# Kernel tuning notes

Measured on AMD Instinct MI355X. Metric: run time of the kernel, lower is better.

## Reference

```python
import jax, jax.numpy as jnp
import numpy as np

D_MODEL = 1024
NUM_HEADS = 16
D_HEAD = D_MODEL // NUM_HEADS
B, T = 2, 2048


def setup_inputs() -> dict:
    key = jax.random.key(0)
    kx, kq, kk, kv, ko = jax.random.split(key, 5)
    # xavier_uniform bound for square (D,D) linear weights
    bound = float(np.sqrt(6.0 / (D_MODEL + D_MODEL)))
    uni = lambda k: jax.random.uniform(k, (D_MODEL, D_MODEL), jnp.float32, -bound, bound)
    return {
        "x": jax.random.normal(kx, (B, T, D_MODEL), jnp.float32),
        "Wq": uni(kq),
        "Wk": uni(kk),
        "Wv": uni(kv),
        "Wo": uni(ko),
    }


def _split_heads(x):
    # (B, T, D) -> (B, H, T, d_head)
    b, t, _ = x.shape
    return x.reshape(b, t, NUM_HEADS, D_HEAD).transpose(0, 2, 1, 3)


def _exclusive_output_mod(Y, V):
    dt = V.dtype
    tiny = jnp.asarray(jnp.finfo(dt).tiny, dt)
    eps = jnp.asarray(jnp.finfo(dt).eps, dt)
    v_sq = jnp.sum(V * V, axis=-1, keepdims=True)
    y_dot_v = jnp.sum(Y * V, axis=-1, keepdims=True)
    scale = jnp.where(v_sq > 0, y_dot_v / jnp.maximum(v_sq, tiny), jnp.zeros_like(y_dot_v))
    Z = Y - scale * V
    residual_norm = jnp.linalg.norm(Z, axis=-1, keepdims=True)
    reference_norm = jnp.maximum(
        jnp.linalg.norm(Y, axis=-1, keepdims=True),
        jnp.linalg.norm(V, axis=-1, keepdims=True),
    )
    cleanup_tol = eps * Z.shape[-1] * reference_norm
    return jnp.where((v_sq > 0) & (residual_norm <= cleanup_tol), jnp.zeros_like(Z), Z)


def reference(x, Wq, Wk, Wv, Wo):
    Q = _split_heads(x @ Wq.T)  # (B,H,T,dh)
    K = _split_heads(x @ Wk.T)
    V = _split_heads(x @ Wv.T)
    sm_scale = 1.0 / np.sqrt(D_HEAD)
    scores = jnp.einsum("bhqd,bhkd->bhqk", Q, K) * sm_scale
    P = jax.nn.softmax(scores, axis=-1)
    Y = jnp.einsum("bhqk,bhkd->bhqd", P, V)
    Z = _exclusive_output_mod(Y, V)
    # merge heads: (B,H,T,dh) -> (B,T,D)
    Zm = Z.transpose(0, 2, 1, 3).reshape(x.shape[0], x.shape[1], D_MODEL)
    return Zm @ Wo.T
```

## Files before the change

### kernel.cpp

```cpp
#include <hip/hip_runtime.h>
#include <math.h>

#define DM   1024
#define TTOK 2048
#define NTOK 4096

typedef __bf16 bf16x8 __attribute__((ext_vector_type(8)));
typedef __bf16 bf16x4 __attribute__((ext_vector_type(4)));
typedef float  f32x4  __attribute__((ext_vector_type(4)));

#define QSCALE 0.18033688011112042f

#if defined(__has_builtin)
#if __has_builtin(__builtin_amdgcn_exp2f)
#define EXP2F(x) __builtin_amdgcn_exp2f(x)
#endif
#endif
#ifndef EXP2F
#define EXP2F(x) exp2f(x)
#endif

#define GLDS16(g, l) __builtin_amdgcn_global_load_lds( \
    (__attribute__((address_space(1))) void*)(g),      \
    (__attribute__((address_space(3))) void*)(l), 16, 0, 0)

__device__ __forceinline__ float qsum(float v) {
    v += __shfl_xor(v, 16, 64);
    v += __shfl_xor(v, 32, 64);
    return v;
}

__global__ __launch_bounds__(256)
void cvt_all(const float* __restrict__ x,  const float* __restrict__ Wq,
             const float* __restrict__ Wk, const float* __restrict__ Wv,
             const float* __restrict__ Wo, __bf16* __restrict__ dst) {
    size_t g = ((size_t)blockIdx.x * 256 + threadIdx.x) * 8;
    const float* s;
    size_t off;
    const size_t NX = (size_t)NTOK * DM;
    if (g < NX) { s = x; off = g; }
    else {
        size_t gg = g - NX;
        int w = (int)(gg >> 20);
        off = gg & ((1u << 20) - 1);
        s = (w == 0) ? Wq : (w == 1) ? Wk : (w == 2) ? Wv : Wo;
        off += 0;
    }
    float4 a = *(const float4*)(s + off);
    float4 b = *(const float4*)(s + off + 4);
    bf16x8 v;
    v[0] = (__bf16)a.x; v[1] = (__bf16)a.y; v[2] = (__bf16)a.z; v[3] = (__bf16)a.w;
    v[4] = (__bf16)b.x; v[5] = (__bf16)b.y; v[6] = (__bf16)b.z; v[7] = (__bf16)b.w;
    *(bf16x8*)(dst + g) = v;
}

template<int MODE>
__global__ __launch_bounds__(256)
void gemm_bf16(const __bf16* __restrict__ A,
               const __bf16* __restrict__ W0, const __bf16* __restrict__ W1,
               const __bf16* __restrict__ W2,
               __bf16* __restrict__ Oq, __bf16* __restrict__ Ok,
               __bf16* __restrict__ Ovt, float* __restrict__ Of)
{
    const int z = (MODE == 0) ? blockIdx.z : 0;
    const __bf16* W = (z == 0) ? W0 : (z == 1) ? W1 : W2;

    __shared__ __attribute__((aligned(16))) __bf16 As[128 * 32];
    __shared__ __attribute__((aligned(16))) __bf16 Bs[128 * 32];

    const int tid  = threadIdx.x;
    const int lane = tid & 63;
    const int wave = tid >> 6;
    const int wm = wave & 1, wn = wave >> 1;
    const int col = lane & 15, quad = lane >> 4;
    const int m0 = blockIdx.y * 128, n0 = blockIdx.x * 128;

    const __bf16* Ag = A + (size_t)(m0 + (tid >> 2)) * DM + (tid & 3) * 8;
    const __bf16* Wg = W + (size_t)(n0 + (tid >> 2)) * DM + (tid & 3) * 8;
    __bf16* lA = As + tid * 8;
    __bf16* lB = Bs + tid * 8;

    f32x4 acc[4][4];
#pragma unroll
    for (int i = 0; i < 4; ++i)
#pragma unroll
        for (int j = 0; j < 4; ++j)
#pragma unroll
            for (int r = 0; r < 4; ++r) acc[i][j][r] = 0.0f;

    for (int k0 = 0; k0 < DM; k0 += 32) {
        __syncthreads();
        GLDS16(Ag + k0,                   lA);
        GLDS16(Ag + (size_t)64 * DM + k0, lA + 2048);
        GLDS16(Wg + k0,                   lB);
        GLDS16(Wg + (size_t)64 * DM + k0, lB + 2048);
        __syncthreads();
        bf16x8 af[4], bfr[4];
#pragma unroll
        for (int i = 0; i < 4; ++i)
            af[i] = *(const bf16x8*)&As[(wm * 64 + i * 16 + col) * 32 + quad * 8];
#pragma unroll
        for (int j = 0; j < 4; ++j)
            bfr[j] = *(const bf16x8*)&Bs[(wn * 64 + j * 16 + col) * 32 + quad * 8];
#pragma unroll
        for (int i = 0; i < 4; ++i)
#pragma unroll
            for (int j = 0; j < 4; ++j)
                acc[i][j] = __builtin_amdgcn_mfma_f32_16x16x32_bf16(af[i], bfr[j], acc[i][j], 0, 0, 0);
    }

#pragma unroll
    for (int i = 0; i < 4; ++i) {
#pragma unroll
        for (int j = 0; j < 4; ++j) {
            const int mb = m0 + wm * 64 + i * 16 + quad * 4;
            const int n  = n0 + wn * 64 + j * 16 + col;
            if (MODE == 1) {
#pragma unroll
                for (int r = 0; r < 4; ++r)
                    Of[(size_t)(mb + r) * DM + n] = acc[i][j][r];
            } else {
                const int b = mb >> 11, t = mb & 2047;
                const int h = n >> 6,  d = n & 63;
                if (z == 2) {
                    bf16x4 pk;
#pragma unroll
                    for (int r = 0; r < 4; ++r) pk[r] = (__bf16)acc[i][j][r];
                    *(bf16x4*)&Ovt[(((size_t)(b * 16 + h)) * 64 + d) * TTOK + t] = pk;
                } else {
                    __bf16* dst = ((z == 0) ? Oq : Ok) +
                                  ((((size_t)(b * 16 + h)) * TTOK + t) * 64 + d);
                    const float sc = (z == 0) ? QSCALE : 1.0f;
#pragma unroll
                    for (int r = 0; r < 4; ++r) dst[(size_t)r * 64] = (__bf16)(acc[i][j][r] * sc);
                }
            }
        }
    }
}

__global__ __launch_bounds__(512)
void attn_mfma(const __bf16* __restrict__ Qg, const __bf16* __restrict__ Kg,
               const __bf16* __restrict__ Vtg, __bf16* __restrict__ Zm)
{
    const int bh = blockIdx.y;
    const int q0 = blockIdx.x * 128;
    const size_t base = (size_t)bh * TTOK * 64;

    __shared__ __attribute__((aligned(16))) __bf16 Ks[64 * 72];
    __shared__ __attribute__((aligned(16))) __bf16 Vs[64 * 72];
    __shared__ __attribute__((aligned(16))) __bf16 QPs[128 * 72];

    const int tid  = threadIdx.x;
    const int lane = tid & 63, wave = tid >> 6;
    const int col  = lane & 15, quad = lane >> 4;

#pragma unroll
    for (int it = 0; it < 2; ++it) {
        int c = tid + 512 * it;
        int r = c >> 3, off = (c & 7) * 8;
        *(bf16x8*)&QPs[r * 72 + off] =
            *(const bf16x8*)(Qg + base + (size_t)(q0 + r) * 64 + off);
    }
    __syncthreads();
    bf16x8 qf[2];
#pragma unroll
    for (int ks = 0; ks < 2; ++ks)
        qf[ks] = *(const bf16x8*)&QPs[(wave * 16 + col) * 72 + ks * 32 + quad * 8];

    bf16x8 ones;
#pragma unroll
    for (int i = 0; i < 8; ++i) ones[i] = (__bf16)1.0f;

    f32x4 O[4], lacc;
#pragma unroll
    for (int r = 0; r < 4; ++r) {
        lacc[r] = 0.0f;
#pragma unroll
        for (int nd = 0; nd < 4; ++nd) O[nd][r] = 0.0f;
    }

    const int rs = tid >> 3, offs = (tid & 7) * 8;

    for (int kb = 0; kb < TTOK / 64; ++kb) {
        bf16x8 kreg = *(const bf16x8*)(Kg + base + (size_t)(kb * 64 + rs) * 64 + offs);
        bf16x8 vreg = *(const bf16x8*)(Vtg + base + (size_t)rs * TTOK + kb * 64 + offs);
        __syncthreads();
        *(bf16x8*)&Ks[rs * 72 + offs] = kreg;
        *(bf16x8*)&Vs[rs * 72 + offs] = vreg;
        __syncthreads();

        f32x4 s[4];
#pragma unroll
        for (int nk = 0; nk < 4; ++nk)
#pragma unroll
            for (int r = 0; r < 4; ++r) s[nk][r] = 0.0f;
#pragma unroll
        for (int ks = 0; ks < 2; ++ks) {
            bf16x8 kf[4];
#pragma unroll
            for (int nk = 0; nk < 4; ++nk)
                kf[nk] = *(const bf16x8*)&Ks[(nk * 16 + col) * 72 + ks * 32 + quad * 8];
#pragma unroll
            for (int nk = 0; nk < 4; ++nk)
                s[nk] = __builtin_amdgcn_mfma_f32_16x16x32_bf16(kf[nk], qf[ks], s[nk], 0, 0, 0);
        }

#pragma unroll
        for (int nk = 0; nk < 4; ++nk) {
            float p0 = EXP2F(s[nk][0]);
            float p1 = EXP2F(s[nk][1]);
            float p2 = EXP2F(s[nk][2]);
            float p3 = EXP2F(s[nk][3]);
            bf16x4 pk;
            pk[0] = (__bf16)p0; pk[1] = (__bf16)p1;
            pk[2] = (__bf16)p2; pk[3] = (__bf16)p3;
            *(bf16x4*)&QPs[(wave * 16 + col) * 72 + nk * 16 + quad * 4] = pk;
        }

#pragma unroll
        for (int ks = 0; ks < 2; ++ks) {
            bf16x8 pf = *(const bf16x8*)&QPs[(wave * 16 + col) * 72 + ks * 32 + quad * 8];
            lacc = __builtin_amdgcn_mfma_f32_16x16x32_bf16(ones, pf, lacc, 0, 0, 0);
#pragma unroll
            for (int nd = 0; nd < 4; ++nd) {
                bf16x8 vf = *(const bf16x8*)&Vs[(nd * 16 + col) * 72 + ks * 32 + quad * 8];
                O[nd] = __builtin_amdgcn_mfma_f32_16x16x32_bf16(vf, pf, O[nd], 0, 0, 0);
            }
        }
    }

    const float inv = 1.0f / lacc[0];

    const int b = bh >> 4, h = bh & 15;
    const int q = q0 + wave * 16 + col;
    float y[4][4], vq[4][4];
    float yv = 0.f, v2 = 0.f, yy = 0.f;
#pragma unroll
    for (int nd = 0; nd < 4; ++nd)
#pragma unroll
        for (int r = 0; r < 4; ++r) {
            int d = nd * 16 + quad * 4 + r;
            float yval = O[nd][r] * inv;
            float vval = (float)Vtg[base + (size_t)d * TTOK + q];
            y[nd][r] = yval; vq[nd][r] = vval;
            yv += yval * vval; v2 += vval * vval; yy += yval * yval;
        }
    yv = qsum(yv); v2 = qsum(v2); yy = qsum(yy);
    float scl = (v2 > 0.0f) ? yv / fmaxf(v2, 1.1754943508222875e-38f) : 0.0f;
    float zz = 0.f;
    float zv[4][4];
#pragma unroll
    for (int nd = 0; nd < 4; ++nd)
#pragma unroll
        for (int r = 0; r < 4; ++r) {
            zv[nd][r] = y[nd][r] - scl * vq[nd][r];
            zz += zv[nd][r] * zv[nd][r];
        }
    zz = qsum(zz);
    float znorm = sqrtf(zz);
    float refn  = fmaxf(sqrtf(yy), sqrtf(v2));
    bool  wipe  = (v2 > 0.0f) && (znorm <= 1.1920928955078125e-07f * 64.0f * refn);
#pragma unroll
    for (int nd = 0; nd < 4; ++nd) {
        bf16x4 pk;
#pragma unroll
        for (int r = 0; r < 4; ++r) pk[r] = (__bf16)(wipe ? 0.0f : zv[nd][r]);
        *(bf16x4*)&Zm[((size_t)(b * TTOK + q)) * DM + h * 64 + nd * 16 + quad * 4] = pk;
    }
}

extern "C" void kernel_launch(void* const* d_in, const int* in_sizes, int n_in,
                              void* d_out, int out_size, void* d_ws, size_t ws_size,
                              hipStream_t stream) {
    const float* x  = (const float*)d_in[0];
    const float* Wq = (const float*)d_in[1];
    const float* Wk = (const float*)d_in[2];
    const float* Wv = (const float*)d_in[3];
    const float* Wo = (const float*)d_in[4];

    const size_t NX = (size_t)NTOK * DM;
    const size_t NW = (size_t)DM * DM;
    __bf16* xb  = (__bf16*)d_ws;
    __bf16* wqb = xb  + NX;
    __bf16* wkb = wqb + NW;
    __bf16* wvb = wkb + NW;
    __bf16* wob = wvb + NW;
    __bf16* Qb  = wob + NW;
    __bf16* Kb  = Qb  + NX;
    __bf16* Vtb = Kb  + NX;
    __bf16* Zmb = Vtb + NX;

    cvt_all<<<(NX + 4 * NW) / 2048, 256, 0, stream>>>(x, Wq, Wk, Wv, Wo, xb);

    gemm_bf16<0><<<dim3(DM / 128, NTOK / 128, 3), 256, 0, stream>>>(
        xb, wqb, wkb, wvb, Qb, Kb, Vtb, nullptr);

    attn_mfma<<<dim3(TTOK / 128, 32), 512, 0, stream>>>(Qb, Kb, Vtb, Zmb);

    gemm_bf16<1><<<dim3(DM / 128, NTOK / 128, 1), 256, 0, stream>>>(
        Zmb, wob, wob, wob, nullptr, nullptr, nullptr, (float*)d_out);
}
```

Before: 200.1 us.

## Switch attention to 32x32 MFMA with K/V prefetch and swap GEMM operands

The attention kernel moves from 16x16x32 to 32x32x16 bf16 MFMA, with 4 waves of 32 query rows each instead of 8 waves of 16. It register-prefetches the next K/V tile during compute, and it captures each query's own V row from shared memory when that tile passes, replacing a strided global gather in the epilogue. The Q/K projection and output GEMMs swap operands so the weight matrix is the M side, which gives contiguous vector stores (bf16x4 and float4) in place of scattered scalar stores. The risks are higher register pressure from the f32x16 accumulators and lower occupancy with the smaller block.

Measured after the change: 209.3 us. 1.05x slower.

```diff
diff --git a/kernel.cpp b/kernel.cpp
--- a/kernel.cpp
+++ b/kernel.cpp
@@ -8,6 +8,7 @@
 typedef __bf16 bf16x8 __attribute__((ext_vector_type(8)));
 typedef __bf16 bf16x4 __attribute__((ext_vector_type(4)));
 typedef float  f32x4  __attribute__((ext_vector_type(4)));
+typedef float  f32x16 __attribute__((ext_vector_type(16)));
 
 #define QSCALE 0.18033688011112042f
 
@@ -23,12 +24,6 @@
 #define GLDS16(g, l) __builtin_amdgcn_global_load_lds( \
     (__attribute__((address_space(1))) void*)(g),      \
     (__attribute__((address_space(3))) void*)(l), 16, 0, 0)
-
-__device__ __forceinline__ float qsum(float v) {
-    v += __shfl_xor(v, 16, 64);
-    v += __shfl_xor(v, 32, 64);
-    return v;
-}
 
 __global__ __launch_bounds__(256)
 void cvt_all(const float* __restrict__ x,  const float* __restrict__ Wq,
@@ -44,7 +39,6 @@
         int w = (int)(gg >> 20);
         off = gg & ((1u << 20) - 1);
         s = (w == 0) ? Wq : (w == 1) ? Wk : (w == 2) ? Wv : Wo;
-        off += 0;
     }
     float4 a = *(const float4*)(s + off);
     float4 b = *(const float4*)(s + off + 4);
@@ -56,14 +50,25 @@
 
 template<int MODE>
 __global__ __launch_bounds__(256)
-void gemm_bf16(const __bf16* __restrict__ A,
+void gemm_bf16(const __bf16* __restrict__ X,
                const __bf16* __restrict__ W0, const __bf16* __restrict__ W1,
                const __bf16* __restrict__ W2,
                __bf16* __restrict__ Oq, __bf16* __restrict__ Ok,
                __bf16* __restrict__ Ovt, float* __restrict__ Of)
 {
-    const int z = (MODE == 0) ? blockIdx.z : 0;
-    const __bf16* W = (z == 0) ? W0 : (z == 1) ? W1 : W2;
+    const int z = (MODE == 0) ? blockIdx.z : 3;
+    const __bf16 *A, *B;
+    int m0, n0;
+    if (MODE == 0 && z < 2) {
+        A = z ? W1 : W0; B = X;
+        m0 = blockIdx.y * 128; n0 = blockIdx.x * 128;
+    } else if (MODE == 0) {
+        A = X; B = W2;
+        m0 = blockIdx.x * 128; n0 = blockIdx.y * 128;
+    } else {
+        A = W0; B = X;
+        m0 = blockIdx.y * 128; n0 = blockIdx.x * 128;
+    }
 
     __shared__ __attribute__((aligned(16))) __bf16 As[128 * 32];
     __shared__ __attribute__((aligned(16))) __bf16 Bs[128 * 32];
@@ -73,10 +78,9 @@
     const int wave = tid >> 6;
     const int wm = wave & 1, wn = wave >> 1;
     const int col = lane & 15, quad = lane >> 4;
-    const int m0 = blockIdx.y * 128, n0 = blockIdx.x * 128;
 
     const __bf16* Ag = A + (size_t)(m0 + (tid >> 2)) * DM + (tid & 3) * 8;
-    const __bf16* Wg = W + (size_t)(n0 + (tid >> 2)) * DM + (tid & 3) * 8;
+    const __bf16* Bg = B + (size_t)(n0 + (tid >> 2)) * DM + (tid & 3) * 8;
     __bf16* lA = As + tid * 8;
     __bf16* lB = Bs + tid * 8;
 
@@ -92,8 +96,8 @@
         __syncthreads();
         GLDS16(Ag + k0,                   lA);
         GLDS16(Ag + (size_t)64 * DM + k0, lA + 2048);
-        GLDS16(Wg + k0,                   lB);
-        GLDS16(Wg + (size_t)64 * DM + k0, lB + 2048);
+        GLDS16(Bg + k0,                   lB);
+        GLDS16(Bg + (size_t)64 * DM + k0, lB + 2048);
         __syncthreads();
         bf16x8 af[4], bfr[4];
 #pragma unroll
@@ -116,30 +120,30 @@
             const int mb = m0 + wm * 64 + i * 16 + quad * 4;
             const int n  = n0 + wn * 64 + j * 16 + col;
             if (MODE == 1) {
-#pragma unroll
-                for (int r = 0; r < 4; ++r)
-                    Of[(size_t)(mb + r) * DM + n] = acc[i][j][r];
+                float4 st = make_float4(acc[i][j][0], acc[i][j][1],
+                                        acc[i][j][2], acc[i][j][3]);
+                *(float4*)&Of[(size_t)n * DM + mb] = st;
+            } else if (z < 2) {
+                const int h = mb >> 6, d = mb & 63;
+                const int b = n >> 11, t = n & 2047;
+                const float sc = z ? 1.0f : QSCALE;
+                bf16x4 pk;
+#pragma unroll
+                for (int r = 0; r < 4; ++r) pk[r] = (__bf16)(acc[i][j][r] * sc);
+                *(bf16x4*)&((z ? Ok : Oq)[(((size_t)(b * 16 + h)) * TTOK + t) * 64 + d]) = pk;
             } else {
                 const int b = mb >> 11, t = mb & 2047;
                 const int h = n >> 6,  d = n & 63;
-                if (z == 2) {
-                    bf16x4 pk;
-#pragma unroll
-                    for (int r = 0; r < 4; ++r) pk[r] = (__bf16)acc[i][j][r];
-                    *(bf16x4*)&Ovt[(((size_t)(b * 16 + h)) * 64 + d) * TTOK + t] = pk;
-                } else {
-                    __bf16* dst = ((z == 0) ? Oq : Ok) +
-                                  ((((size_t)(b * 16 + h)) * TTOK + t) * 64 + d);
-                    const float sc = (z == 0) ? QSCALE : 1.0f;
-#pragma unroll
-                    for (int r = 0; r < 4; ++r) dst[(size_t)r * 64] = (__bf16)(acc[i][j][r] * sc);
-                }
+                bf16x4 pk;
+#pragma unroll
+                for (int r = 0; r < 4; ++r) pk[r] = (__bf16)acc[i][j][r];
+                *(bf16x4*)&Ovt[(((size_t)(b * 16 + h)) * 64 + d) * TTOK + t] = pk;
             }
         }
     }
 }
 
-__global__ __launch_bounds__(512)
+__global__ __launch_bounds__(256)
 void attn_mfma(const __bf16* __restrict__ Qg, const __bf16* __restrict__ Kg,
                const __bf16* __restrict__ Vtg, __bf16* __restrict__ Zm)
 {
@@ -153,121 +157,147 @@
 
     const int tid  = threadIdx.x;
     const int lane = tid & 63, wave = tid >> 6;
-    const int col  = lane & 15, quad = lane >> 4;
+    const int c32  = lane & 31, h32 = lane >> 5;
 
 #pragma unroll
     for (int it = 0; it < 2; ++it) {
-        int c = tid + 512 * it;
-        int r = c >> 3, off = (c & 7) * 8;
-        *(bf16x8*)&QPs[r * 72 + off] =
-            *(const bf16x8*)(Qg + base + (size_t)(q0 + r) * 64 + off);
+        int idx = tid + 256 * it;
+        int r = idx >> 2, off = (idx & 3) * 16;
+        const __bf16* src = Qg + base + (size_t)(q0 + r) * 64 + off;
+        *(bf16x8*)&QPs[r * 72 + off]     = *(const bf16x8*)(src);
+        *(bf16x8*)&QPs[r * 72 + off + 8] = *(const bf16x8*)(src + 8);
     }
     __syncthreads();
-    bf16x8 qf[2];
-#pragma unroll
-    for (int ks = 0; ks < 2; ++ks)
-        qf[ks] = *(const bf16x8*)&QPs[(wave * 16 + col) * 72 + ks * 32 + quad * 8];
+    bf16x8 qf[4];
+#pragma unroll
+    for (int st = 0; st < 4; ++st)
+        qf[st] = *(const bf16x8*)&QPs[(wave * 32 + c32) * 72 + h32 * 8 + st * 16];
 
     bf16x8 ones;
 #pragma unroll
     for (int i = 0; i < 8; ++i) ones[i] = (__bf16)1.0f;
 
-    f32x4 O[4], lacc;
-#pragma unroll
-    for (int r = 0; r < 4; ++r) {
-        lacc[r] = 0.0f;
-#pragma unroll
-        for (int nd = 0; nd < 4; ++nd) O[nd][r] = 0.0f;
-    }
-
-    const int rs = tid >> 3, offs = (tid & 7) * 8;
+    f32x16 O[2], lacc;
+#pragma unroll
+    for (int r = 0; r < 16; ++r) { O[0][r] = 0.0f; O[1][r] = 0.0f; lacc[r] = 0.0f; }
+
+    const int rs = tid >> 2, soff = (tid & 3) * 16;
+
+    bf16x8 kr0 = *(const bf16x8*)(Kg  + base + (size_t)rs * 64 + soff);
+    bf16x8 kr1 = *(const bf16x8*)(Kg  + base + (size_t)rs * 64 + soff + 8);
+    bf16x8 vr0 = *(const bf16x8*)(Vtg + base + (size_t)rs * TTOK + soff);
+    bf16x8 vr1 = *(const bf16x8*)(Vtg + base + (size_t)rs * TTOK + soff + 8);
+
+    const int kb_tgt = (q0 >> 6) + (wave >> 1);
+    const int qo     = (wave & 1) * 32 + c32;
+    float vq[2][16];
 
     for (int kb = 0; kb < TTOK / 64; ++kb) {
-        bf16x8 kreg = *(const bf16x8*)(Kg + base + (size_t)(kb * 64 + rs) * 64 + offs);
-        bf16x8 vreg = *(const bf16x8*)(Vtg + base + (size_t)rs * TTOK + kb * 64 + offs);
         __syncthreads();
-        *(bf16x8*)&Ks[rs * 72 + offs] = kreg;
-        *(bf16x8*)&Vs[rs * 72 + offs] = vreg;
+        *(bf16x8*)&Ks[rs * 72 + soff]     = kr0;
+        *(bf16x8*)&Ks[rs * 72 + soff + 8] = kr1;
+        *(bf16x8*)&Vs[rs * 72 + soff]     = vr0;
+        *(bf16x8*)&Vs[rs * 72 + soff + 8] = vr1;
         __syncthreads();
 
-        f32x4 s[4];
-#pragma unroll
-        for (int nk = 0; nk < 4; ++nk)
-#pragma unroll
-            for (int r = 0; r < 4; ++r) s[nk][r] = 0.0f;
-#pragma unroll
-        for (int ks = 0; ks < 2; ++ks) {
-            bf16x8 kf[4];
-#pragma unroll
-            for (int nk = 0; nk < 4; ++nk)
-                kf[nk] = *(const bf16x8*)&Ks[(nk * 16 + col) * 72 + ks * 32 + quad * 8];
-#pragma unroll
-            for (int nk = 0; nk < 4; ++nk)
-                s[nk] = __builtin_amdgcn_mfma_f32_16x16x32_bf16(kf[nk], qf[ks], s[nk], 0, 0, 0);
-        }
-
-#pragma unroll
-        for (int nk = 0; nk < 4; ++nk) {
-            float p0 = EXP2F(s[nk][0]);
-            float p1 = EXP2F(s[nk][1]);
-            float p2 = EXP2F(s[nk][2]);
-            float p3 = EXP2F(s[nk][3]);
-            bf16x4 pk;
-            pk[0] = (__bf16)p0; pk[1] = (__bf16)p1;
-            pk[2] = (__bf16)p2; pk[3] = (__bf16)p3;
-            *(bf16x4*)&QPs[(wave * 16 + col) * 72 + nk * 16 + quad * 4] = pk;
-        }
-
-#pragma unroll
-        for (int ks = 0; ks < 2; ++ks) {
-            bf16x8 pf = *(const bf16x8*)&QPs[(wave * 16 + col) * 72 + ks * 32 + quad * 8];
-            lacc = __builtin_amdgcn_mfma_f32_16x16x32_bf16(ones, pf, lacc, 0, 0, 0);
-#pragma unroll
-            for (int nd = 0; nd < 4; ++nd) {
-                bf16x8 vf = *(const bf16x8*)&Vs[(nd * 16 + col) * 72 + ks * 32 + quad * 8];
-                O[nd] = __builtin_amdgcn_mfma_f32_16x16x32_bf16(vf, pf, O[nd], 0, 0, 0);
+        {
+            int kbn = (kb + 1) & (TTOK / 64 - 1);
+            const __bf16* kp = Kg  + base + (size_t)(kbn * 64 + rs) * 64 + soff;
+            const __bf16* vp = Vtg + base + (size_t)rs * TTOK + kbn * 64 + soff;
+            kr0 = *(const bf16x8*)(kp); kr1 = *(const bf16x8*)(kp + 8);
+            vr0 = *(const bf16x8*)(vp); vr1 = *(const bf16x8*)(vp + 8);
+        }
+
+        f32x16 s0, s1;
+#pragma unroll
+        for (int r = 0; r < 16; ++r) { s0[r] = 0.0f; s1[r] = 0.0f; }
+#pragma unroll
+        for (int st = 0; st < 4; ++st) {
+            bf16x8 a0 = *(const bf16x8*)&Ks[(c32)      * 72 + h32 * 8 + st * 16];
+            bf16x8 a1 = *(const bf16x8*)&Ks[(32 + c32) * 72 + h32 * 8 + st * 16];
+            s0 = __builtin_amdgcn_mfma_f32_32x32x16_bf16(a0, qf[st], s0, 0, 0, 0);
+            s1 = __builtin_amdgcn_mfma_f32_32x32x16_bf16(a1, qf[st], s1, 0, 0, 0);
+        }
+
+#pragma unroll
+        for (int kb2 = 0; kb2 < 2; ++kb2) {
+#pragma unroll
+            for (int g = 0; g < 4; ++g) {
+                float p0 = EXP2F(kb2 ? s1[4 * g + 0] : s0[4 * g + 0]);
+                float p1 = EXP2F(kb2 ? s1[4 * g + 1] : s0[4 * g + 1]);
+                float p2 = EXP2F(kb2 ? s1[4 * g + 2] : s0[4 * g + 2]);
+                float p3 = EXP2F(kb2 ? s1[4 * g + 3] : s0[4 * g + 3]);
+                bf16x4 pk;
+                pk[0] = (__bf16)p0; pk[1] = (__bf16)p1;
+                pk[2] = (__bf16)p2; pk[3] = (__bf16)p3;
+                *(bf16x4*)&QPs[(wave * 32 + c32) * 72 + kb2 * 32 + g * 8 + h32 * 4] = pk;
             }
         }
+
+#pragma unroll
+        for (int ks = 0; ks < 4; ++ks) {
+            bf16x8 pf = *(const bf16x8*)&QPs[(wave * 32 + c32) * 72 + h32 * 8 + ks * 16];
+            lacc = __builtin_amdgcn_mfma_f32_32x32x16_bf16(ones, pf, lacc, 0, 0, 0);
+            bf16x8 v0 = *(const bf16x8*)&Vs[(c32)      * 72 + h32 * 8 + ks * 16];
+            bf16x8 v1 = *(const bf16x8*)&Vs[(32 + c32) * 72 + h32 * 8 + ks * 16];
+            O[0] = __builtin_amdgcn_mfma_f32_32x32x16_bf16(v0, pf, O[0], 0, 0, 0);
+            O[1] = __builtin_amdgcn_mfma_f32_32x32x16_bf16(v1, pf, O[1], 0, 0, 0);
+        }
+
+        if (kb == kb_tgt) {
+#pragma unroll
+            for (int db = 0; db < 2; ++db)
+#pragma unroll
+                for (int rg = 0; rg < 16; ++rg) {
+                    int d = db * 32 + (rg & 3) + 8 * (rg >> 2) + 4 * h32;
+                    vq[db][rg] = (float)Vs[d * 72 + qo];
+                }
+        }
     }
 
     const float inv = 1.0f / lacc[0];
 
     const int b = bh >> 4, h = bh & 15;
-    const int q = q0 + wave * 16 + col;
-    float y[4][4], vq[4][4];
+    const int q = q0 + wave * 32 + c32;
+    float y[2][16];
     float yv = 0.f, v2 = 0.f, yy = 0.f;
 #pragma unroll
-    for (int nd = 0; nd < 4; ++nd)
-#pragma unroll
-        for (int r = 0; r < 4; ++r) {
-            int d = nd * 16 + quad * 4 + r;
-            float yval = O[nd][r] * inv;
-            float vval = (float)Vtg[base + (size_t)d * TTOK + q];
-            y[nd][r] = yval; vq[nd][r] = vval;
+    for (int db = 0; db < 2; ++db)
+#pragma unroll
+        for (int rg = 0; rg < 16; ++rg) {
+            float yval = O[db][rg] * inv;
+            float vval = vq[db][rg];
+            y[db][rg] = yval;
             yv += yval * vval; v2 += vval * vval; yy += yval * yval;
         }
-    yv = qsum(yv); v2 = qsum(v2); yy = qsum(yy);
+    yv += __shfl_xor(yv, 32, 64);
+    v2 += __shfl_xor(v2, 32, 64);
+    yy += __shfl_xor(yy, 32, 64);
     float scl = (v2 > 0.0f) ? yv / fmaxf(v2, 1.1754943508222875e-38f) : 0.0f;
     float zz = 0.f;
-    float zv[4][4];
-#pragma unroll
-    for (int nd = 0; nd < 4; ++nd)
-#pragma unroll
-        for (int r = 0; r < 4; ++r) {
-            zv[nd][r] = y[nd][r] - scl * vq[nd][r];
-            zz += zv[nd][r] * zv[nd][r];
-        }
-    zz = qsum(zz);
+    float zvv[2][16];
+#pragma unroll
+    for (int db = 0; db < 2; ++db)
+#pragma unroll
+        for (int rg = 0; rg < 16; ++rg) {
+            zvv[db][rg] = y[db][rg] - scl * vq[db][rg];
+            zz += zvv[db][rg] * zvv[db][rg];
+        }
+    zz += __shfl_xor(zz, 32, 64);
     float znorm = sqrtf(zz);
     float refn  = fmaxf(sqrtf(yy), sqrtf(v2));
     bool  wipe  = (v2 > 0.0f) && (znorm <= 1.1920928955078125e-07f * 64.0f * refn);
 #pragma unroll
-    for (int nd = 0; nd < 4; ++nd) {
-        bf16x4 pk;
-#pragma unroll
-        for (int r = 0; r < 4; ++r) pk[r] = (__bf16)(wipe ? 0.0f : zv[nd][r]);
-        *(bf16x4*)&Zm[((size_t)(b * TTOK + q)) * DM + h * 64 + nd * 16 + quad * 4] = pk;
-    }
+    for (int db = 0; db < 2; ++db)
+#pragma unroll
+        for (int g = 0; g < 4; ++g) {
+            bf16x4 pk;
+#pragma unroll
+            for (int r = 0; r < 4; ++r)
+                pk[r] = (__bf16)(wipe ? 0.0f : zvv[db][4 * g + r]);
+            int d = db * 32 + 8 * g + 4 * h32;
+            *(bf16x4*)&Zm[((size_t)(b * TTOK + q)) * DM + h * 64 + d] = pk;
+        }
 }
 
 extern "C" void kernel_launch(void* const* d_in, const int* in_sizes, int n_in,
@@ -293,11 +323,11 @@
 
     cvt_all<<<(NX + 4 * NW) / 2048, 256, 0, stream>>>(x, Wq, Wk, Wv, Wo, xb);
 
-    gemm_bf16<0><<<dim3(DM / 128, NTOK / 128, 3), 256, 0, stream>>>(
+    gemm_bf16<0><<<dim3(32, 8, 3), 256, 0, stream>>>(
         xb, wqb, wkb, wvb, Qb, Kb, Vtb, nullptr);
 
-    attn_mfma<<<dim3(TTOK / 128, 32), 512, 0, stream>>>(Qb, Kb, Vtb, Zmb);
-
-    gemm_bf16<1><<<dim3(DM / 128, NTOK / 128, 1), 256, 0, stream>>>(
-        Zmb, wob, wob, wob, nullptr, nullptr, nullptr, (float*)d_out);
+    attn_mfma<<<dim3(TTOK / 128, 32), 256, 0, stream>>>(Qb, Kb, Vtb, Zmb);
+
+    gemm_bf16<1><<<dim3(32, 8, 1), 256, 0, stream>>>(
+        Zmb, wob, nullptr, nullptr, nullptr, nullptr, nullptr, (float*)d_out);
 }
```
